# Kernel tuning notes

Measured on AMD Instinct MI355X. Metric: run time of the kernel, lower is better.

Reference implementation:

```python
import jax, jax.numpy as jnp
import numpy as np

TEMPERATURE = 8.0  # sqrt(d_k) with d_k = 64
NEG_INF = -jnp.inf


def setup_inputs() -> dict:
    key = jax.random.key(0)
    kq, kk, kv = jax.random.split(key, 3)
    b, n, d = 16, 2048, 64
    q = jax.random.normal(kq, (b, n, d), dtype=jnp.float32)
    k = jax.random.normal(kk, (b, n, d), dtype=jnp.float32)
    v = jax.random.normal(kv, (b, n, d), dtype=jnp.float32)
    # causal mask: True where attention is disallowed (strict upper triangle)
    mask = jnp.broadcast_to(jnp.triu(jnp.ones((n, n), dtype=bool), k=1), (b, n, n))
    return {"q": q, "k": k, "v": v, "mask": mask}


def reference(q, k, v, mask):
    # attn = q @ k^T / temperature   [b, n, n]
    attn = jnp.einsum('bqd,bkd->bqk', q, k) / TEMPERATURE
    attn = jnp.where(mask, NEG_INF, attn)
    attn = jax.nn.softmax(attn, axis=2)
    # output = attn @ v   [b, n, d]
    output = jnp.einsum('bqk,bkd->bqd', attn, v)
    return (output, attn)
```

## Files before the change

kernel.cpp:

```cpp
#include <hip/hip_runtime.h>


constexpr int B = 16;
constexpr int N = 2048;
constexpr int D = 64;
constexpr float INV_TEMP = 0.125f;

typedef __attribute__((ext_vector_type(8))) short bf16x8;
typedef __attribute__((ext_vector_type(4))) float f32x4;

__device__ __forceinline__ short f2bf(float f) {
    __bf16 h = (__bf16)f;
    return __builtin_bit_cast(short, h);
}

__global__ __launch_bounds__(256) void sdpa_mfma(
    const float* __restrict__ q,
    const float* __restrict__ k,
    const float* __restrict__ v,
    float* __restrict__ out,
    float* __restrict__ attn)
{
    const int x = blockIdx.x;
    const int b = x >> 5;
    const int u = x & 31;
    const int qt = (u & 1) ? (31 - (u >> 1)) : (u >> 1);
    const int qs = qt * 64;

    const int t    = threadIdx.x;
    const int w    = t >> 6;
    const int lane = t & 63;
    const int l15  = lane & 15;
    const int quad = lane >> 4;
    const int q8   = quad * 8;

    __shared__ __align__(16) short sK[64][72];
    __shared__ __align__(16) short sV[64][72];
    __shared__ __align__(16) short sP[4][16][72];

    const float* qb = q + (size_t)b * N * D;
    const float* kb = k + (size_t)b * N * D;
    const float* vb = v + (size_t)b * N * D;
    float* attn_b = attn + (size_t)b * N * N;

    const int srow = t >> 2;
    const int sd   = (t & 3) * 16;

    {
        const int ce = (qt + 1) * 64;
        float4 z = {0.f, 0.f, 0.f, 0.f};
        float* arow = attn_b + (size_t)(qs + srow) * N;
        for (int c = ce + (t & 3) * 16; c < N; c += 64) {
            float4* p4 = (float4*)(arow + c);
            p4[0] = z; p4[1] = z; p4[2] = z; p4[3] = z;
        }
    }

    {
        const float4* src = (const float4*)(qb + (size_t)(qs + srow) * D + sd);
        float4 f0 = src[0], f1 = src[1], f2 = src[2], f3 = src[3];
        float vals[16] = {f0.x,f0.y,f0.z,f0.w, f1.x,f1.y,f1.z,f1.w,
                          f2.x,f2.y,f2.z,f2.w, f3.x,f3.y,f3.z,f3.w};
        short* dst = &sK[srow][sd];
#pragma unroll
        for (int i = 0; i < 16; ++i) dst[i] = f2bf(vals[i]);
    }
    __syncthreads();
    const bf16x8 qa0 = *(const bf16x8*)&sK[w * 16 + l15][q8];
    const bf16x8 qa1 = *(const bf16x8*)&sK[w * 16 + l15][32 + q8];

    float rs[4] = {0.f, 0.f, 0.f, 0.f};
    for (int kt = 0; kt <= qt; ++kt) {
        __syncthreads();
        {
            const float4* src = (const float4*)(kb + (size_t)(kt * 64 + srow) * D + sd);
            float4 f0 = src[0], f1 = src[1], f2 = src[2], f3 = src[3];
            float vals[16] = {f0.x,f0.y,f0.z,f0.w, f1.x,f1.y,f1.z,f1.w,
                              f2.x,f2.y,f2.z,f2.w, f3.x,f3.y,f3.z,f3.w};
            short* dst = &sK[srow][sd];
#pragma unroll
            for (int i = 0; i < 16; ++i) dst[i] = f2bf(vals[i]);
        }
        __syncthreads();
        const bool diag = (kt == qt);
#pragma unroll
        for (int nt = 0; nt < 4; ++nt) {
            bf16x8 b0 = *(const bf16x8*)&sK[nt * 16 + l15][q8];
            bf16x8 b1 = *(const bf16x8*)&sK[nt * 16 + l15][32 + q8];
            f32x4 c = {0.f, 0.f, 0.f, 0.f};
            c = __builtin_amdgcn_mfma_f32_16x16x32_bf16(qa0, b0, c, 0, 0, 0);
            c = __builtin_amdgcn_mfma_f32_16x16x32_bf16(qa1, b1, c, 0, 0, 0);
            const int col = nt * 16 + l15;
#pragma unroll
            for (int r = 0; r < 4; ++r) {
                const int rowl = w * 16 + quad * 4 + r;
                float p = (!diag || col <= rowl) ? __expf(c[r] * INV_TEMP) : 0.f;
                rs[r] += p;
            }
        }
    }

    float inv[4];
#pragma unroll
    for (int r = 0; r < 4; ++r) {
        float s = rs[r];
        s += __shfl_xor(s, 1);
        s += __shfl_xor(s, 2);
        s += __shfl_xor(s, 4);
        s += __shfl_xor(s, 8);
        inv[r] = 1.f / s;
    }

    f32x4 o[4];
#pragma unroll
    for (int nt = 0; nt < 4; ++nt) o[nt] = {0.f, 0.f, 0.f, 0.f};

    for (int kt = 0; kt <= qt; ++kt) {
        __syncthreads();
        {
            const float4* src = (const float4*)(kb + (size_t)(kt * 64 + srow) * D + sd);
            float4 f0 = src[0], f1 = src[1], f2 = src[2], f3 = src[3];
            float vals[16] = {f0.x,f0.y,f0.z,f0.w, f1.x,f1.y,f1.z,f1.w,
                              f2.x,f2.y,f2.z,f2.w, f3.x,f3.y,f3.z,f3.w};
            short* dst = &sK[srow][sd];
#pragma unroll
            for (int i = 0; i < 16; ++i) dst[i] = f2bf(vals[i]);
        }
        {
            const float4* src = (const float4*)(vb + (size_t)(kt * 64 + srow) * D + sd);
            float4 f0 = src[0], f1 = src[1], f2 = src[2], f3 = src[3];
            float vals[16] = {f0.x,f0.y,f0.z,f0.w, f1.x,f1.y,f1.z,f1.w,
                              f2.x,f2.y,f2.z,f2.w, f3.x,f3.y,f3.z,f3.w};
#pragma unroll
            for (int i = 0; i < 16; ++i) sV[sd + i][srow] = f2bf(vals[i]);
        }
        __syncthreads();
        const bool diag = (kt == qt);
#pragma unroll
        for (int nt = 0; nt < 4; ++nt) {
            bf16x8 b0 = *(const bf16x8*)&sK[nt * 16 + l15][q8];
            bf16x8 b1 = *(const bf16x8*)&sK[nt * 16 + l15][32 + q8];
            f32x4 c = {0.f, 0.f, 0.f, 0.f};
            c = __builtin_amdgcn_mfma_f32_16x16x32_bf16(qa0, b0, c, 0, 0, 0);
            c = __builtin_amdgcn_mfma_f32_16x16x32_bf16(qa1, b1, c, 0, 0, 0);
            const int col = nt * 16 + l15;
            float* arow = attn_b + (size_t)(qs + w * 16 + quad * 4) * N + kt * 64 + col;
#pragma unroll
            for (int r = 0; r < 4; ++r) {
                const int rowl = w * 16 + quad * 4 + r;
                float p = (!diag || col <= rowl) ? __expf(c[r] * INV_TEMP) * inv[r] : 0.f;
                arow[(size_t)r * N] = p;
                sP[w][quad * 4 + r][col] = f2bf(p);
            }
        }
#pragma unroll
        for (int kc = 0; kc < 2; ++kc) {
            bf16x8 a = *(const bf16x8*)&sP[w][l15][kc * 32 + q8];
#pragma unroll
            for (int nt = 0; nt < 4; ++nt) {
                bf16x8 vf = *(const bf16x8*)&sV[nt * 16 + l15][kc * 32 + q8];
                o[nt] = __builtin_amdgcn_mfma_f32_16x16x32_bf16(a, vf, o[nt], 0, 0, 0);
            }
        }
    }

#pragma unroll
    for (int nt = 0; nt < 4; ++nt) {
        float* orow = out + (size_t)(b * N + qs + w * 16 + quad * 4) * D + nt * 16 + l15;
#pragma unroll
        for (int r = 0; r < 4; ++r) orow[(size_t)r * D] = o[nt][r];
    }
}

extern "C" void kernel_launch(void* const* d_in, const int* in_sizes, int n_in,
                              void* d_out, int out_size, void* d_ws, size_t ws_size,
                              hipStream_t stream) {
    const float* q = (const float*)d_in[0];
    const float* k = (const float*)d_in[1];
    const float* v = (const float*)d_in[2];

    float* out  = (float*)d_out;
    float* attn = out + (size_t)B * N * D;

    sdpa_mfma<<<dim3(B * 32), dim3(256), 0, stream>>>(q, k, v, out, attn);
}
```

Before: 507.2 us.

## Fuse softmax into single pass by buffering unnormalized probabilities in LDS

Replaces the two-pass scheme (one pass for row sums, one recomputing QK^T to write normalized attention) with a single pass. Unnormalized bf16 probabilities for a 32-row tile are kept in a large LDS buffer, and P@V is accumulated unnormalized. Rows are normalized at the end, and the full attention rows, including zeros past the causal band, are written with coalesced float4 stores. It also moves to 512-thread blocks covering 32 query rows, register-prefetches the next K/V tile, and uses vectorized LDS stores. The cost is about 140KB of dynamic LDS per block, which limits occupancy, and row sums now accumulate bf16-rounded values.

```diff
diff --git a/kernel.cpp b/kernel.cpp
--- a/kernel.cpp
+++ b/kernel.cpp
@@ -6,26 +6,47 @@
 constexpr int D = 64;
 constexpr float INV_TEMP = 0.125f;
 
+constexpr int RS = 2056;
+constexpr int SP_BYTES  = 32 * RS * 2;
+constexpr int SK_OFF    = SP_BYTES;
+constexpr int SV_OFF    = SK_OFF + 64 * 72 * 2;
+constexpr int RSUM_OFF  = SV_OFF + 64 * 72 * 2;
+constexpr int SINV_OFF  = RSUM_OFF + 8 * 16 * 4;
+constexpr int SMEM_BYTES = SINV_OFF + 32 * 4;
+
 typedef __attribute__((ext_vector_type(8))) short bf16x8;
+typedef __attribute__((ext_vector_type(4))) short bf16x4;
 typedef __attribute__((ext_vector_type(4))) float f32x4;
 
 __device__ __forceinline__ short f2bf(float f) {
     __bf16 h = (__bf16)f;
     return __builtin_bit_cast(short, h);
 }
-
-__global__ __launch_bounds__(256) void sdpa_mfma(
+__device__ __forceinline__ float bf2f(short s) {
+    unsigned int u = ((unsigned int)(unsigned short)s) << 16;
+    return __builtin_bit_cast(float, u);
+}
+
+__global__ __launch_bounds__(512) void sdpa_fused(
     const float* __restrict__ q,
     const float* __restrict__ k,
     const float* __restrict__ v,
     float* __restrict__ out,
     float* __restrict__ attn)
 {
+    extern __shared__ __align__(16) char smem[];
+    short (*sP)[RS] = reinterpret_cast<short(*)[RS]>(smem);
+    short (*sK)[72] = reinterpret_cast<short(*)[72]>(smem + SK_OFF);
+    short (*sV)[72] = reinterpret_cast<short(*)[72]>(smem + SV_OFF);
+    float* rsum = reinterpret_cast<float*>(smem + RSUM_OFF);
+    float* sinv = reinterpret_cast<float*>(smem + SINV_OFF);
+
     const int x = blockIdx.x;
-    const int b = x >> 5;
-    const int u = x & 31;
-    const int qt = (u & 1) ? (31 - (u >> 1)) : (u >> 1);
-    const int qs = qt * 64;
+    const int b = x >> 6;
+    const int u = x & 63;
+    const int rt = 63 - u;
+    const int qs = rt * 32;
+    const int ntiles = (rt >> 1) + 1;
 
     const int t    = threadIdx.x;
     const int w    = t >> 6;
@@ -33,74 +54,87 @@
     const int l15  = lane & 15;
     const int quad = lane >> 4;
     const int q8   = quad * 8;
-
-    __shared__ __align__(16) short sK[64][72];
-    __shared__ __align__(16) short sV[64][72];
-    __shared__ __align__(16) short sP[4][16][72];
+    const int rg   = w & 1;
+    const int cg   = w >> 1;
 
     const float* qb = q + (size_t)b * N * D;
     const float* kb = k + (size_t)b * N * D;
     const float* vb = v + (size_t)b * N * D;
     float* attn_b = attn + (size_t)b * N * N;
 
-    const int srow = t >> 2;
-    const int sd   = (t & 3) * 16;
+    const int krow = t >> 3;
+    const int kc8  = (t & 7) * 8;
+
+    float4 kf0, kf1;
+    float  vr[8];
 
     {
-        const int ce = (qt + 1) * 64;
-        float4 z = {0.f, 0.f, 0.f, 0.f};
-        float* arow = attn_b + (size_t)(qs + srow) * N;
-        for (int c = ce + (t & 3) * 16; c < N; c += 64) {
-            float4* p4 = (float4*)(arow + c);
-            p4[0] = z; p4[1] = z; p4[2] = z; p4[3] = z;
-        }
-    }
-
-    {
-        const float4* src = (const float4*)(qb + (size_t)(qs + srow) * D + sd);
-        float4 f0 = src[0], f1 = src[1], f2 = src[2], f3 = src[3];
-        float vals[16] = {f0.x,f0.y,f0.z,f0.w, f1.x,f1.y,f1.z,f1.w,
-                          f2.x,f2.y,f2.z,f2.w, f3.x,f3.y,f3.z,f3.w};
-        short* dst = &sK[srow][sd];
-#pragma unroll
-        for (int i = 0; i < 16; ++i) dst[i] = f2bf(vals[i]);
+        const float4* s = (const float4*)(kb + (size_t)krow * D + kc8);
+        kf0 = s[0]; kf1 = s[1];
+        const float* sv = vb + (size_t)(w * 8) * D + lane;
+#pragma unroll
+        for (int i = 0; i < 8; ++i) vr[i] = sv[(size_t)i * D];
+    }
+
+    if (t < 256) {
+        const float4* s = (const float4*)(qb + (size_t)(qs + krow) * D + kc8);
+        float4 a = s[0], c4 = s[1];
+        float qv[8] = {a.x,a.y,a.z,a.w, c4.x,c4.y,c4.z,c4.w};
+        bf16x8 pq;
+#pragma unroll
+        for (int i = 0; i < 8; ++i) pq[i] = f2bf(qv[i]);
+        *(bf16x8*)&sK[krow][kc8] = pq;
     }
     __syncthreads();
-    const bf16x8 qa0 = *(const bf16x8*)&sK[w * 16 + l15][q8];
-    const bf16x8 qa1 = *(const bf16x8*)&sK[w * 16 + l15][32 + q8];
+    const bf16x8 qa0 = *(const bf16x8*)&sK[rg * 16 + l15][q8];
+    const bf16x8 qa1 = *(const bf16x8*)&sK[rg * 16 + l15][32 + q8];
 
     float rs[4] = {0.f, 0.f, 0.f, 0.f};
-    for (int kt = 0; kt <= qt; ++kt) {
+    f32x4 o = {0.f, 0.f, 0.f, 0.f};
+
+    for (int kt = 0; kt < ntiles; ++kt) {
         __syncthreads();
         {
-            const float4* src = (const float4*)(kb + (size_t)(kt * 64 + srow) * D + sd);
-            float4 f0 = src[0], f1 = src[1], f2 = src[2], f3 = src[3];
-            float vals[16] = {f0.x,f0.y,f0.z,f0.w, f1.x,f1.y,f1.z,f1.w,
-                              f2.x,f2.y,f2.z,f2.w, f3.x,f3.y,f3.z,f3.w};
-            short* dst = &sK[srow][sd];
-#pragma unroll
-            for (int i = 0; i < 16; ++i) dst[i] = f2bf(vals[i]);
+            float kv[8] = {kf0.x,kf0.y,kf0.z,kf0.w, kf1.x,kf1.y,kf1.z,kf1.w};
+            bf16x8 pk, pv;
+#pragma unroll
+            for (int i = 0; i < 8; ++i) pk[i] = f2bf(kv[i]);
+#pragma unroll
+            for (int i = 0; i < 8; ++i) pv[i] = f2bf(vr[i]);
+            *(bf16x8*)&sK[krow][kc8]  = pk;
+            *(bf16x8*)&sV[lane][w*8]  = pv;
         }
         __syncthreads();
-        const bool diag = (kt == qt);
-#pragma unroll
-        for (int nt = 0; nt < 4; ++nt) {
-            bf16x8 b0 = *(const bf16x8*)&sK[nt * 16 + l15][q8];
-            bf16x8 b1 = *(const bf16x8*)&sK[nt * 16 + l15][32 + q8];
-            f32x4 c = {0.f, 0.f, 0.f, 0.f};
-            c = __builtin_amdgcn_mfma_f32_16x16x32_bf16(qa0, b0, c, 0, 0, 0);
-            c = __builtin_amdgcn_mfma_f32_16x16x32_bf16(qa1, b1, c, 0, 0, 0);
-            const int col = nt * 16 + l15;
-#pragma unroll
-            for (int r = 0; r < 4; ++r) {
-                const int rowl = w * 16 + quad * 4 + r;
-                float p = (!diag || col <= rowl) ? __expf(c[r] * INV_TEMP) : 0.f;
-                rs[r] += p;
-            }
-        }
-    }
-
-    float inv[4];
+        if (kt + 1 < ntiles) {
+            const float4* s = (const float4*)(kb + (size_t)((kt+1)*64 + krow) * D + kc8);
+            kf0 = s[0]; kf1 = s[1];
+            const float* sv = vb + (size_t)((kt+1)*64 + w*8) * D + lane;
+#pragma unroll
+            for (int i = 0; i < 8; ++i) vr[i] = sv[(size_t)i * D];
+        }
+        bf16x8 kb0 = *(const bf16x8*)&sK[cg * 16 + l15][q8];
+        bf16x8 kb1 = *(const bf16x8*)&sK[cg * 16 + l15][32 + q8];
+        f32x4 c = {0.f, 0.f, 0.f, 0.f};
+        c = __builtin_amdgcn_mfma_f32_16x16x32_bf16(qa0, kb0, c, 0, 0, 0);
+        c = __builtin_amdgcn_mfma_f32_16x16x32_bf16(qa1, kb1, c, 0, 0, 0);
+        const int colg = kt * 64 + cg * 16 + l15;
+#pragma unroll
+        for (int r = 0; r < 4; ++r) {
+            const int rowg = qs + rg * 16 + quad * 4 + r;
+            float pr = (colg <= rowg) ? __expf(c[r] * INV_TEMP) : 0.f;
+            short sp = f2bf(pr);
+            rs[r] += bf2f(sp);
+            sP[rg * 16 + quad * 4 + r][kt * 64 + cg * 16 + l15] = sp;
+        }
+        __syncthreads();
+#pragma unroll
+        for (int kc = 0; kc < 2; ++kc) {
+            bf16x8 a  = *(const bf16x8*)&sP[rg * 16 + l15][kt * 64 + kc * 32 + q8];
+            bf16x8 vf = *(const bf16x8*)&sV[cg * 16 + l15][kc * 32 + q8];
+            o = __builtin_amdgcn_mfma_f32_16x16x32_bf16(a, vf, o, 0, 0, 0);
+        }
+    }
+
 #pragma unroll
     for (int r = 0; r < 4; ++r) {
         float s = rs[r];
@@ -108,67 +142,44 @@
         s += __shfl_xor(s, 2);
         s += __shfl_xor(s, 4);
         s += __shfl_xor(s, 8);
-        inv[r] = 1.f / s;
-    }
-
-    f32x4 o[4];
-#pragma unroll
-    for (int nt = 0; nt < 4; ++nt) o[nt] = {0.f, 0.f, 0.f, 0.f};
-
-    for (int kt = 0; kt <= qt; ++kt) {
-        __syncthreads();
-        {
-            const float4* src = (const float4*)(kb + (size_t)(kt * 64 + srow) * D + sd);
-            float4 f0 = src[0], f1 = src[1], f2 = src[2], f3 = src[3];
-            float vals[16] = {f0.x,f0.y,f0.z,f0.w, f1.x,f1.y,f1.z,f1.w,
-                              f2.x,f2.y,f2.z,f2.w, f3.x,f3.y,f3.z,f3.w};
-            short* dst = &sK[srow][sd];
-#pragma unroll
-            for (int i = 0; i < 16; ++i) dst[i] = f2bf(vals[i]);
-        }
-        {
-            const float4* src = (const float4*)(vb + (size_t)(kt * 64 + srow) * D + sd);
-            float4 f0 = src[0], f1 = src[1], f2 = src[2], f3 = src[3];
-            float vals[16] = {f0.x,f0.y,f0.z,f0.w, f1.x,f1.y,f1.z,f1.w,
-                              f2.x,f2.y,f2.z,f2.w, f3.x,f3.y,f3.z,f3.w};
-#pragma unroll
-            for (int i = 0; i < 16; ++i) sV[sd + i][srow] = f2bf(vals[i]);
-        }
-        __syncthreads();
-        const bool diag = (kt == qt);
-#pragma unroll
-        for (int nt = 0; nt < 4; ++nt) {
-            bf16x8 b0 = *(const bf16x8*)&sK[nt * 16 + l15][q8];
-            bf16x8 b1 = *(const bf16x8*)&sK[nt * 16 + l15][32 + q8];
-            f32x4 c = {0.f, 0.f, 0.f, 0.f};
-            c = __builtin_amdgcn_mfma_f32_16x16x32_bf16(qa0, b0, c, 0, 0, 0);
-            c = __builtin_amdgcn_mfma_f32_16x16x32_bf16(qa1, b1, c, 0, 0, 0);
-            const int col = nt * 16 + l15;
-            float* arow = attn_b + (size_t)(qs + w * 16 + quad * 4) * N + kt * 64 + col;
-#pragma unroll
-            for (int r = 0; r < 4; ++r) {
-                const int rowl = w * 16 + quad * 4 + r;
-                float p = (!diag || col <= rowl) ? __expf(c[r] * INV_TEMP) * inv[r] : 0.f;
-                arow[(size_t)r * N] = p;
-                sP[w][quad * 4 + r][col] = f2bf(p);
-            }
-        }
-#pragma unroll
-        for (int kc = 0; kc < 2; ++kc) {
-            bf16x8 a = *(const bf16x8*)&sP[w][l15][kc * 32 + q8];
-#pragma unroll
-            for (int nt = 0; nt < 4; ++nt) {
-                bf16x8 vf = *(const bf16x8*)&sV[nt * 16 + l15][kc * 32 + q8];
-                o[nt] = __builtin_amdgcn_mfma_f32_16x16x32_bf16(a, vf, o[nt], 0, 0, 0);
-            }
-        }
-    }
-
-#pragma unroll
-    for (int nt = 0; nt < 4; ++nt) {
-        float* orow = out + (size_t)(b * N + qs + w * 16 + quad * 4) * D + nt * 16 + l15;
-#pragma unroll
-        for (int r = 0; r < 4; ++r) orow[(size_t)r * D] = o[nt][r];
+        rs[r] = s;
+    }
+    if (l15 == 0) {
+#pragma unroll
+        for (int r = 0; r < 4; ++r) rsum[w * 16 + quad * 4 + r] = rs[r];
+    }
+    __syncthreads();
+    if (t < 32) {
+        const int rg2 = t >> 4, rl = t & 15;
+        float tot = rsum[(rg2 + 0) * 16 + rl] + rsum[(rg2 + 2) * 16 + rl]
+                  + rsum[(rg2 + 4) * 16 + rl] + rsum[(rg2 + 6) * 16 + rl];
+        sinv[t] = 1.f / tot;
+    }
+    __syncthreads();
+
+#pragma unroll
+    for (int r = 0; r < 4; ++r) {
+        const int rowl = rg * 16 + quad * 4 + r;
+        out[(size_t)(b * N + qs + rowl) * D + cg * 16 + l15] = o[r] * sinv[rowl];
+    }
+
+    const int erow = t >> 4;
+    const int ec   = (t & 15) * 4;
+    const float einv = sinv[erow];
+    float* arow = attn_b + (size_t)(qs + erow) * N;
+    const int lim = ntiles * 64;
+    for (int c0 = ec; c0 < N; c0 += 64) {
+        float4 f;
+        if (c0 < lim) {
+            bf16x4 p4 = *(const bf16x4*)&sP[erow][c0];
+            f.x = bf2f(p4[0]) * einv;
+            f.y = bf2f(p4[1]) * einv;
+            f.z = bf2f(p4[2]) * einv;
+            f.w = bf2f(p4[3]) * einv;
+        } else {
+            f = {0.f, 0.f, 0.f, 0.f};
+        }
+        *(float4*)(arow + c0) = f;
     }
 }
 
@@ -182,5 +193,13 @@
     float* out  = (float*)d_out;
     float* attn = out + (size_t)B * N * D;
 
-    sdpa_mfma<<<dim3(B * 32), dim3(256), 0, stream>>>(q, k, v, out, attn);
-}
+    static bool attr_set = false;
+    if (!attr_set) {
+        (void)hipFuncSetAttribute((const void*)sdpa_fused,
+                                  hipFuncAttributeMaxDynamicSharedMemorySize,
+                                  SMEM_BYTES);
+        attr_set = true;
+    }
+
+    sdpa_fused<<<dim3(B * 64), dim3(512), SMEM_BYTES, stream>>>(q, k, v, out, attn);
+}
```

Measured after the change: 514.1 us. Within noise of the previous version (+1.4%).
